# Kernel optimization log

Measured on AMD Instinct MI355X. Metric: run time of the kernel, lower is better.

The kernel has to match this reference:

```python
import jax, jax.numpy as jnp
import numpy as np

B, D, T_STEPS = 256, 512, 256


def setup_inputs() -> dict:
    key = jax.random.key(0)
    k1, k2 = jax.random.split(key)
    # Scale K like flax lecun_normal init (std = 1/sqrt(fan_in)) so rollout stays stable.
    z0 = jax.random.normal(k1, (B, D), dtype=jnp.float32)
    K = jax.random.normal(k2, (D, D), dtype=jnp.float32) / np.sqrt(D)
    return {"z0": z0, "K": K, "T": T_STEPS}


def reference(z0, K, T):
    # z_{t+1} = z_t @ K  (flax Linear with use_bias=False: y = x @ kernel)
    def step(z, _):
        z_next = z @ K  # [B, D] @ [D, D] -> [B, D]
        return z_next, z_next

    _, preds = jax.lax.scan(step, z0, xs=None, length=T)  # [T, B, D]
    return jnp.transpose(preds, (1, 0, 2))  # [B, T, D]
```

## Files before the change

### kernel.cpp

```cpp
#include <hip/hip_runtime.h>


typedef unsigned short u16;
typedef unsigned int u32;
typedef __bf16 bf16x8 __attribute__((ext_vector_type(8)));
typedef float f32x4 __attribute__((ext_vector_type(4)));
typedef u16 u16x4 __attribute__((ext_vector_type(4)));

#define MAT 262144
#define SLOT 1048576
#define WSLOT 131072

static_assert(sizeof(bf16x8) == 16, "bf16x8 must be 16B");

__device__ __forceinline__ u16 f2b(float f) {
  u32 x = __float_as_uint(f);
  return (u16)((x + 0x7fffu + ((x >> 16) & 1u)) >> 16);
}
__device__ __forceinline__ float b2f(u16 u) { return __uint_as_float(((u32)u) << 16); }

__device__ __forceinline__ void gll16(const void* g, void* l) {
  __builtin_amdgcn_global_load_lds((__attribute__((address_space(1))) void*)(void*)g,
                                   (__attribute__((address_space(3))) void*)l, 16, 0, 0);
}

__global__ __launch_bounds__(256) void prep_kernel(const float* __restrict__ Kc,
                                                   const float* __restrict__ z0,
                                                   u16* __restrict__ P,
                                                   u16* __restrict__ W0,
                                                   u16* __restrict__ z0lo) {
  __shared__ float tile[64][65];
  int tid = threadIdx.x, b = blockIdx.x;
  if (b < 64) {
    int by = b >> 3, bx = b & 7;
#pragma unroll 4
    for (int q = 0; q < 16; ++q) {
      int lin = q * 256 + tid;
      int r = lin >> 6, c = lin & 63;
      float v = Kc[(size_t)(by * 64 + r) * 512 + bx * 64 + c];
      tile[r][c] = v;
      u16 h = f2b(v), l = f2b(v - b2f(h));
      size_t o = (size_t)(by * 64 + r) * 512 + bx * 64 + c;
      P[o] = h;
      P[MAT + o] = l;
    }
    __syncthreads();
#pragma unroll 4
    for (int q = 0; q < 16; ++q) {
      int lin = q * 256 + tid;
      int c = lin >> 6, r = lin & 63;
      float v = tile[r][c];
      u16 h = f2b(v), l = f2b(v - b2f(h));
      size_t o = (size_t)(bx * 64 + c) * 512 + by * 64 + r;
      P[2 * MAT + o] = h;
      P[3 * MAT + o] = l;
    }
  } else {
    int idb = b - 64;
#pragma unroll 4
    for (int q = 0; q < 16; ++q) {
      int id = (idb * 16 + q) * 256 + tid;
      float v = z0[id];
      u16 h = f2b(v);
      W0[id] = h;
      z0lo[id] = f2b(v - b2f(h));
    }
  }
}

__global__ __launch_bounds__(256) void gemm_split(
    const u16* __restrict__ A0h, const u16* __restrict__ A0l, long Astr,
    const u16* __restrict__ B0h, long Bstr,
    u16* __restrict__ C0, long Cstr, int wmode) {
  __shared__ u16 Ah_s[64 * 32], Al_s[64 * 32], Bh_s[64 * 32], Bl_s[64 * 32];
  int z = blockIdx.z;
  const u16* Ah = A0h + (size_t)z * Astr;
  const u16* Al = A0l + (size_t)z * Astr;
  const u16* Bh = B0h + (size_t)z * Bstr;
  const u16* Bl = Bh + MAT;
  u16* C = C0 + (size_t)z * Cstr;
  int tid = threadIdx.x;
  int m0 = blockIdx.y * 64, n0 = blockIdx.x * 64;
  int lrow = tid >> 2, lc4 = tid & 3;
  size_t aoff = (size_t)(m0 + lrow) * 512 + lc4 * 8;
  size_t boff = (size_t)(n0 + lrow) * 512 + lc4 * 8;
  int wv = tid >> 6, lane = tid & 63;
  int lb = wv * 512;
  int wm = wv >> 1, wn = wv & 1, mrow = lane & 15, quad = lane >> 4;
  int aro = (wm * 32 + mrow) * 32 + quad * 8;
  int bro = (wn * 32 + mrow) * 32 + quad * 8;
  f32x4 acc[2][2] = {};
  for (int kt = 0; kt < 16; ++kt) {
    int ko = kt * 32;
    gll16(Ah + aoff + ko, Ah_s + lb);
    gll16(Al + aoff + ko, Al_s + lb);
    gll16(Bh + boff + ko, Bh_s + lb);
    gll16(Bl + boff + ko, Bl_s + lb);
    __syncthreads();
    bf16x8 ah[2], al[2], bh[2], bl[2];
#pragma unroll
    for (int t2 = 0; t2 < 2; ++t2) {
      ah[t2] = *(const bf16x8*)(Ah_s + aro + t2 * 16 * 32);
      al[t2] = *(const bf16x8*)(Al_s + aro + t2 * 16 * 32);
      bh[t2] = *(const bf16x8*)(Bh_s + bro + t2 * 16 * 32);
      bl[t2] = *(const bf16x8*)(Bl_s + bro + t2 * 16 * 32);
    }
#pragma unroll
    for (int mt = 0; mt < 2; ++mt)
#pragma unroll
      for (int nt = 0; nt < 2; ++nt) {
        acc[mt][nt] = __builtin_amdgcn_mfma_f32_16x16x32_bf16(ah[mt], bh[nt], acc[mt][nt], 0, 0, 0);
        acc[mt][nt] = __builtin_amdgcn_mfma_f32_16x16x32_bf16(al[mt], bh[nt], acc[mt][nt], 0, 0, 0);
        acc[mt][nt] = __builtin_amdgcn_mfma_f32_16x16x32_bf16(ah[mt], bl[nt], acc[mt][nt], 0, 0, 0);
      }
    __syncthreads();
  }
#pragma unroll
  for (int mt = 0; mt < 2; ++mt)
#pragma unroll
    for (int nt = 0; nt < 2; ++nt) {
      int mb = m0 + wm * 32 + mt * 16 + quad * 4;
      int nn = n0 + wn * 32 + nt * 16 + mrow;
      if (wmode == 0) {
        u16x4 h4, l4;
#pragma unroll
        for (int r = 0; r < 4; ++r) {
          float v = acc[mt][nt][r];
          u16 h = f2b(v), l = f2b(v - b2f(h));
          C[(size_t)(mb + r) * 512 + nn] = h;
          C[MAT + (size_t)(mb + r) * 512 + nn] = l;
          h4[r] = h;
          l4[r] = l;
        }
        *(u16x4*)(C + 2 * MAT + (size_t)nn * 512 + mb) = h4;
        *(u16x4*)(C + 3 * MAT + (size_t)nn * 512 + mb) = l4;
      } else {
#pragma unroll
        for (int r = 0; r < 4; ++r) C[(size_t)(mb + r) * 512 + nn] = f2b(acc[mt][nt][r]);
      }
    }
}

__global__ __launch_bounds__(256) void gemm_out(const u16* __restrict__ Wb,
                                                const u16* __restrict__ PT0,
                                                float* __restrict__ out) {
  __shared__ u16 As[128 * 32], Bs[128 * 32];
  int z = blockIdx.z;
  const u16* A = Wb + (size_t)(z >> 4) * WSLOT;
  const u16* Bt = PT0 + (size_t)(z & 15) * SLOT;
  int tid = threadIdx.x;
  int m0 = blockIdx.y * 128, n0 = blockIdx.x * 128;
  int lrow = tid >> 2, lc4 = tid & 3;
  size_t aoff = (size_t)(m0 + lrow) * 512 + lc4 * 8;
  size_t boff = (size_t)(n0 + lrow) * 512 + lc4 * 8;
  int wv = tid >> 6, lane = tid & 63;
  int lb = wv * 512;
  int wm = wv >> 1, wn = wv & 1, mrow = lane & 15, quad = lane >> 4;
  int aro = (wm * 64 + mrow) * 32 + quad * 8;
  int bro = (wn * 64 + mrow) * 32 + quad * 8;
  f32x4 acc[4][4] = {};
  for (int kt = 0; kt < 16; ++kt) {
    int ko = kt * 32;
    gll16(A + aoff + ko, As + lb);
    gll16(A + aoff + 64 * 512 + ko, As + 2048 + lb);
    gll16(Bt + boff + ko, Bs + lb);
    gll16(Bt + boff + 64 * 512 + ko, Bs + 2048 + lb);
    __syncthreads();
    bf16x8 a[4], b[4];
#pragma unroll
    for (int t4 = 0; t4 < 4; ++t4) {
      a[t4] = *(const bf16x8*)(As + aro + t4 * 16 * 32);
      b[t4] = *(const bf16x8*)(Bs + bro + t4 * 16 * 32);
    }
#pragma unroll
    for (int mt = 0; mt < 4; ++mt)
#pragma unroll
      for (int nt = 0; nt < 4; ++nt)
        acc[mt][nt] = __builtin_amdgcn_mfma_f32_16x16x32_bf16(a[mt], b[nt], acc[mt][nt], 0, 0, 0);
    __syncthreads();
  }
#pragma unroll
  for (int mt = 0; mt < 4; ++mt)
#pragma unroll
    for (int nt = 0; nt < 4; ++nt) {
      int gb = m0 + wm * 64 + mt * 16 + quad * 4;
      int gd = n0 + wn * 64 + nt * 16 + mrow;
#pragma unroll
      for (int r = 0; r < 4; ++r)
        out[((size_t)(gb + r) * 256 + z) * 512 + gd] = acc[mt][nt][r];
    }
}

extern "C" void kernel_launch(void* const* d_in, const int* in_sizes, int n_in,
                              void* d_out, int out_size, void* d_ws, size_t ws_size,
                              hipStream_t stream) {
  const float* z0 = (const float*)d_in[0];
  const float* Kc = (const float*)d_in[1];
  float* out = (float*)d_out;
  u16* W = (u16*)d_ws;
  u16* z0l = W + 16 * WSLOT;
  u16* P = z0l + WSLOT;
  auto S = [&](int s) { return P + (size_t)s * SLOT; };
  dim3 blk(256);

  prep_kernel<<<96, blk, 0, stream>>>(Kc, z0, P, W, z0l);
  gemm_split<<<dim3(8, 8, 1), blk, 0, stream>>>(S(0), S(0) + MAT, 0, S(0) + 2 * MAT, 0, S(1), 0, 0);
  gemm_split<<<dim3(8, 8, 2), blk, 0, stream>>>(S(0), S(0) + MAT, SLOT, S(1) + 2 * MAT, 0, S(2), SLOT, 0);
  gemm_split<<<dim3(8, 8, 4), blk, 0, stream>>>(S(0), S(0) + MAT, SLOT, S(3) + 2 * MAT, 0, S(4), SLOT, 0);
  gemm_split<<<dim3(8, 8, 8), blk, 0, stream>>>(S(0), S(0) + MAT, SLOT, S(7) + 2 * MAT, 0, S(8), SLOT, 0);
  gemm_split<<<dim3(8, 8, 1), blk, 0, stream>>>(S(15), S(15) + MAT, 0, S(15) + 2 * MAT, 0, S(16), 0, 0);
  gemm_split<<<dim3(8, 8, 2), blk, 0, stream>>>(S(16), S(16) + MAT, 0, S(15) + 2 * MAT, SLOT, S(17), SLOT, 0);
  gemm_split<<<dim3(8, 8, 4), blk, 0, stream>>>(S(18), S(18) + MAT, 0, S(15) + 2 * MAT, SLOT, S(19), SLOT, 0);
  gemm_split<<<dim3(8, 8, 7), blk, 0, stream>>>(S(22), S(22) + MAT, 0, S(15) + 2 * MAT, SLOT, S(23), SLOT, 0);
  gemm_split<<<dim3(8, 4, 15), blk, 0, stream>>>(W, z0l, 0, S(15) + 2 * MAT, SLOT, W + WSLOT, WSLOT, 1);
  gemm_out<<<dim3(4, 2, 256), blk, 0, stream>>>(W, P + 2 * MAT, out);
}
```

Baseline: 289.4 us.

## Store operands in MFMA-fragment-packed layout and load A directly from global

Introduces a packed layout (pidx) in which each 16-row by 32-k chunk is stored contiguously in the order an MFMA fragment reads it. All producers (prep, gemm_split epilogue) now write this layout, and both GEMMs read A fragments straight from global memory as contiguous 16-byte vectors, staging only B in LDS with larger k-groups and fewer barriers. The aim is to cut LDS traffic, synchronisation and uncoalesced accesses. In exchange the epilogue and the transpose stores become scattered 2-byte writes, and A reuse now relies on cache rather than LDS.

```diff
diff --git a/kernel.cpp b/kernel.cpp
--- a/kernel.cpp
+++ b/kernel.cpp
@@ -5,19 +5,20 @@
 typedef unsigned int u32;
 typedef __bf16 bf16x8 __attribute__((ext_vector_type(8)));
 typedef float f32x4 __attribute__((ext_vector_type(4)));
-typedef u16 u16x4 __attribute__((ext_vector_type(4)));
 
 #define MAT 262144
 #define SLOT 1048576
 #define WSLOT 131072
 
-static_assert(sizeof(bf16x8) == 16, "bf16x8 must be 16B");
-
 __device__ __forceinline__ u16 f2b(float f) {
   u32 x = __float_as_uint(f);
   return (u16)((x + 0x7fffu + ((x >> 16) & 1u)) >> 16);
 }
 __device__ __forceinline__ float b2f(u16 u) { return __uint_as_float(((u32)u) << 16); }
+
+__device__ __forceinline__ size_t pidx(int r, int k) {
+  return (size_t)(((r >> 4) * 16 + (k >> 5)) * 512 + ((k >> 3) & 3) * 128 + (r & 15) * 8 + (k & 7));
+}
 
 __device__ __forceinline__ void gll16(const void* g, void* l) {
   __builtin_amdgcn_global_load_lds((__attribute__((address_space(1))) void*)(void*)g,
@@ -29,50 +30,41 @@
                                                    u16* __restrict__ P,
                                                    u16* __restrict__ W0,
                                                    u16* __restrict__ z0lo) {
-  __shared__ float tile[64][65];
   int tid = threadIdx.x, b = blockIdx.x;
   if (b < 64) {
-    int by = b >> 3, bx = b & 7;
+    int r0 = (b >> 3) * 64, c0 = (b & 7) * 64;
 #pragma unroll 4
     for (int q = 0; q < 16; ++q) {
       int lin = q * 256 + tid;
-      int r = lin >> 6, c = lin & 63;
-      float v = Kc[(size_t)(by * 64 + r) * 512 + bx * 64 + c];
-      tile[r][c] = v;
+      int r = r0 + (lin >> 6), c = c0 + (lin & 63);
+      float v = Kc[(size_t)r * 512 + c];
       u16 h = f2b(v), l = f2b(v - b2f(h));
-      size_t o = (size_t)(by * 64 + r) * 512 + bx * 64 + c;
-      P[o] = h;
-      P[MAT + o] = l;
-    }
-    __syncthreads();
-#pragma unroll 4
-    for (int q = 0; q < 16; ++q) {
-      int lin = q * 256 + tid;
-      int c = lin >> 6, r = lin & 63;
-      float v = tile[r][c];
-      u16 h = f2b(v), l = f2b(v - b2f(h));
-      size_t o = (size_t)(bx * 64 + c) * 512 + by * 64 + r;
-      P[2 * MAT + o] = h;
-      P[3 * MAT + o] = l;
+      size_t ia = pidx(r, c), ib = pidx(c, r);
+      P[ia] = h;
+      P[MAT + ia] = l;
+      P[2 * MAT + ib] = h;
+      P[3 * MAT + ib] = l;
     }
   } else {
     int idb = b - 64;
 #pragma unroll 4
     for (int q = 0; q < 16; ++q) {
       int id = (idb * 16 + q) * 256 + tid;
+      int r = id >> 9, c = id & 511;
       float v = z0[id];
       u16 h = f2b(v);
-      W0[id] = h;
-      z0lo[id] = f2b(v - b2f(h));
+      size_t ia = pidx(r, c);
+      W0[ia] = h;
+      z0lo[ia] = f2b(v - b2f(h));
     }
   }
 }
 
-__global__ __launch_bounds__(256) void gemm_split(
+__global__ __launch_bounds__(256, 1) void gemm_split(
     const u16* __restrict__ A0h, const u16* __restrict__ A0l, long Astr,
     const u16* __restrict__ B0h, long Bstr,
     u16* __restrict__ C0, long Cstr, int wmode) {
-  __shared__ u16 Ah_s[64 * 32], Al_s[64 * 32], Bh_s[64 * 32], Bl_s[64 * 32];
+  __shared__ u16 Bs[2][16 * 512];
   int z = blockIdx.z;
   const u16* Ah = A0h + (size_t)z * Astr;
   const u16* Al = A0l + (size_t)z * Astr;
@@ -81,62 +73,69 @@
   u16* C = C0 + (size_t)z * Cstr;
   int tid = threadIdx.x;
   int m0 = blockIdx.y * 64, n0 = blockIdx.x * 64;
-  int lrow = tid >> 2, lc4 = tid & 3;
-  size_t aoff = (size_t)(m0 + lrow) * 512 + lc4 * 8;
-  size_t boff = (size_t)(n0 + lrow) * 512 + lc4 * 8;
   int wv = tid >> 6, lane = tid & 63;
-  int lb = wv * 512;
   int wm = wv >> 1, wn = wv & 1, mrow = lane & 15, quad = lane >> 4;
-  int aro = (wm * 32 + mrow) * 32 + quad * 8;
-  int bro = (wn * 32 + mrow) * 32 + quad * 8;
+  int l8 = lane * 8;
+  int mchunk0 = (m0 >> 4) + wm * 2;
+  int nchunk0 = n0 >> 4;
   f32x4 acc[2][2] = {};
-  for (int kt = 0; kt < 16; ++kt) {
-    int ko = kt * 32;
-    gll16(Ah + aoff + ko, Ah_s + lb);
-    gll16(Al + aoff + ko, Al_s + lb);
-    gll16(Bh + boff + ko, Bh_s + lb);
-    gll16(Bl + boff + ko, Bl_s + lb);
-    __syncthreads();
-    bf16x8 ah[2], al[2], bh[2], bl[2];
-#pragma unroll
-    for (int t2 = 0; t2 < 2; ++t2) {
-      ah[t2] = *(const bf16x8*)(Ah_s + aro + t2 * 16 * 32);
-      al[t2] = *(const bf16x8*)(Al_s + aro + t2 * 16 * 32);
-      bh[t2] = *(const bf16x8*)(Bh_s + bro + t2 * 16 * 32);
-      bl[t2] = *(const bf16x8*)(Bl_s + bro + t2 * 16 * 32);
-    }
-#pragma unroll
-    for (int mt = 0; mt < 2; ++mt)
+  for (int g = 0; g < 4; ++g) {
+#pragma unroll
+    for (int i = 0; i < 8; ++i) {
+      int id = wv * 8 + i;
+      int hl = id >> 4, kt_f = (id >> 2) & 3, nt_loc = id & 3;
+      const u16* src = (hl ? Bl : Bh) + (size_t)((nchunk0 + nt_loc) * 16 + g * 4 + kt_f) * 512 + l8;
+      gll16(src, &Bs[hl][(kt_f * 4 + nt_loc) * 512]);
+    }
+    __syncthreads();
+#pragma unroll
+    for (int kt_f = 0; kt_f < 4; ++kt_f) {
+      int kt = g * 4 + kt_f;
+      bf16x8 ah[2], al[2], bh[2], bl[2];
+#pragma unroll
+      for (int mt = 0; mt < 2; ++mt) {
+        size_t co = (size_t)((mchunk0 + mt) * 16 + kt) * 512 + l8;
+        ah[mt] = *(const bf16x8*)(Ah + co);
+        al[mt] = *(const bf16x8*)(Al + co);
+      }
 #pragma unroll
       for (int nt = 0; nt < 2; ++nt) {
-        acc[mt][nt] = __builtin_amdgcn_mfma_f32_16x16x32_bf16(ah[mt], bh[nt], acc[mt][nt], 0, 0, 0);
-        acc[mt][nt] = __builtin_amdgcn_mfma_f32_16x16x32_bf16(al[mt], bh[nt], acc[mt][nt], 0, 0, 0);
-        acc[mt][nt] = __builtin_amdgcn_mfma_f32_16x16x32_bf16(ah[mt], bl[nt], acc[mt][nt], 0, 0, 0);
+        int slot = kt_f * 4 + wn * 2 + nt;
+        bh[nt] = *(const bf16x8*)(&Bs[0][slot * 512 + l8]);
+        bl[nt] = *(const bf16x8*)(&Bs[1][slot * 512 + l8]);
       }
+#pragma unroll
+      for (int mt = 0; mt < 2; ++mt)
+#pragma unroll
+        for (int nt = 0; nt < 2; ++nt) {
+          acc[mt][nt] = __builtin_amdgcn_mfma_f32_16x16x32_bf16(ah[mt], bh[nt], acc[mt][nt], 0, 0, 0);
+          acc[mt][nt] = __builtin_amdgcn_mfma_f32_16x16x32_bf16(al[mt], bh[nt], acc[mt][nt], 0, 0, 0);
+          acc[mt][nt] = __builtin_amdgcn_mfma_f32_16x16x32_bf16(ah[mt], bl[nt], acc[mt][nt], 0, 0, 0);
+        }
+    }
     __syncthreads();
   }
 #pragma unroll
   for (int mt = 0; mt < 2; ++mt)
 #pragma unroll
     for (int nt = 0; nt < 2; ++nt) {
-      int mb = m0 + wm * 32 + mt * 16 + quad * 4;
-      int nn = n0 + wn * 32 + nt * 16 + mrow;
-      if (wmode == 0) {
-        u16x4 h4, l4;
-#pragma unroll
-        for (int r = 0; r < 4; ++r) {
-          float v = acc[mt][nt][r];
-          u16 h = f2b(v), l = f2b(v - b2f(h));
-          C[(size_t)(mb + r) * 512 + nn] = h;
-          C[MAT + (size_t)(mb + r) * 512 + nn] = l;
-          h4[r] = h;
-          l4[r] = l;
+      int mbase = m0 + wm * 32 + mt * 16 + quad * 4;
+      int n = n0 + wn * 32 + nt * 16 + mrow;
+#pragma unroll
+      for (int r = 0; r < 4; ++r) {
+        int m = mbase + r;
+        float v = acc[mt][nt][r];
+        u16 h = f2b(v);
+        if (wmode == 0) {
+          u16 l = f2b(v - b2f(h));
+          size_t ia = pidx(m, n), ib = pidx(n, m);
+          C[ia] = h;
+          C[MAT + ia] = l;
+          C[2 * MAT + ib] = h;
+          C[3 * MAT + ib] = l;
+        } else {
+          C[pidx(m, n)] = h;
         }
-        *(u16x4*)(C + 2 * MAT + (size_t)nn * 512 + mb) = h4;
-        *(u16x4*)(C + 3 * MAT + (size_t)nn * 512 + mb) = l4;
-      } else {
-#pragma unroll
-        for (int r = 0; r < 4; ++r) C[(size_t)(mb + r) * 512 + nn] = f2b(acc[mt][nt][r]);
       }
     }
 }
@@ -144,39 +143,43 @@
 __global__ __launch_bounds__(256) void gemm_out(const u16* __restrict__ Wb,
                                                 const u16* __restrict__ PT0,
                                                 float* __restrict__ out) {
-  __shared__ u16 As[128 * 32], Bs[128 * 32];
+  __shared__ u16 Bs[16 * 512];
   int z = blockIdx.z;
   const u16* A = Wb + (size_t)(z >> 4) * WSLOT;
   const u16* Bt = PT0 + (size_t)(z & 15) * SLOT;
   int tid = threadIdx.x;
   int m0 = blockIdx.y * 128, n0 = blockIdx.x * 128;
-  int lrow = tid >> 2, lc4 = tid & 3;
-  size_t aoff = (size_t)(m0 + lrow) * 512 + lc4 * 8;
-  size_t boff = (size_t)(n0 + lrow) * 512 + lc4 * 8;
   int wv = tid >> 6, lane = tid & 63;
-  int lb = wv * 512;
   int wm = wv >> 1, wn = wv & 1, mrow = lane & 15, quad = lane >> 4;
-  int aro = (wm * 64 + mrow) * 32 + quad * 8;
-  int bro = (wn * 64 + mrow) * 32 + quad * 8;
+  int l8 = lane * 8;
+  int mchunk0 = (m0 >> 4) + wm * 4;
+  int nchunk0 = n0 >> 4;
   f32x4 acc[4][4] = {};
-  for (int kt = 0; kt < 16; ++kt) {
-    int ko = kt * 32;
-    gll16(A + aoff + ko, As + lb);
-    gll16(A + aoff + 64 * 512 + ko, As + 2048 + lb);
-    gll16(Bt + boff + ko, Bs + lb);
-    gll16(Bt + boff + 64 * 512 + ko, Bs + 2048 + lb);
-    __syncthreads();
-    bf16x8 a[4], b[4];
-#pragma unroll
-    for (int t4 = 0; t4 < 4; ++t4) {
-      a[t4] = *(const bf16x8*)(As + aro + t4 * 16 * 32);
-      b[t4] = *(const bf16x8*)(Bs + bro + t4 * 16 * 32);
-    }
-#pragma unroll
-    for (int mt = 0; mt < 4; ++mt)
+  for (int g = 0; g < 8; ++g) {
+#pragma unroll
+    for (int i = 0; i < 4; ++i) {
+      int id = wv * 4 + i;
+      int kt_f = id >> 3, nt_loc = id & 7;
+      const u16* src = Bt + (size_t)((nchunk0 + nt_loc) * 16 + g * 2 + kt_f) * 512 + l8;
+      gll16(src, &Bs[(kt_f * 8 + nt_loc) * 512]);
+    }
+    __syncthreads();
+#pragma unroll
+    for (int kt_f = 0; kt_f < 2; ++kt_f) {
+      int kt = g * 2 + kt_f;
+      bf16x8 a[4], b[4];
+#pragma unroll
+      for (int mt = 0; mt < 4; ++mt)
+        a[mt] = *(const bf16x8*)(A + (size_t)((mchunk0 + mt) * 16 + kt) * 512 + l8);
 #pragma unroll
       for (int nt = 0; nt < 4; ++nt)
-        acc[mt][nt] = __builtin_amdgcn_mfma_f32_16x16x32_bf16(a[mt], b[nt], acc[mt][nt], 0, 0, 0);
+        b[nt] = *(const bf16x8*)(&Bs[(kt_f * 8 + wn * 4 + nt) * 512 + l8]);
+#pragma unroll
+      for (int mt = 0; mt < 4; ++mt)
+#pragma unroll
+        for (int nt = 0; nt < 4; ++nt)
+          acc[mt][nt] = __builtin_amdgcn_mfma_f32_16x16x32_bf16(a[mt], b[nt], acc[mt][nt], 0, 0, 0);
+    }
     __syncthreads();
   }
 #pragma unroll
```

Result: slower. 305.7 us (+5.7%).
